# Kernel tuning notes

Hardware: AMD Instinct MI355X
Metric: run time of the kernel (lower is better)

## Reference

```python
import jax, jax.numpy as jnp
from jax import lax
import numpy as np

LATENT_DIM = 128
NUM_SAMPLES = 524288
STEPS = 30


def setup_inputs() -> dict:
    key = jax.random.key(0)
    kW, = jax.random.split(key, 1)
    h = jnp.zeros((LATENT_DIM,), dtype=jnp.float32)
    W = jax.random.normal(kW, (LATENT_DIM, LATENT_DIM), dtype=jnp.float32) * 0.001
    return {"h": h, "W": W, "num_samples": NUM_SAMPLES, "steps": STEPS}


def reference(h, W, num_samples, steps):
    # Block Gibbs sampling chain of the RBM: z <- Bernoulli(sigmoid(h + z @ W))
    latent_dim = h.shape[0]
    key = jax.random.key(42)
    k_init, k_loop = jax.random.split(key)
    # initial state: uniform {0,1} bits, matching torch.randint(0, 2, ...)
    z0 = jax.random.randint(k_init, (num_samples, latent_dim), 0, 2).astype(jnp.float32)
    step_keys = jax.random.split(k_loop, steps)

    def gibbs_step(z, k):
        probs = jax.nn.sigmoid(h + z @ W)            # [num_samples, latent_dim]
        u = jax.random.uniform(k, z.shape, dtype=z.dtype)
        z_new = (u < probs).astype(z.dtype)
        return z_new, None

    z_final, _ = lax.scan(gibbs_step, z0, step_keys)
    return z_final
```

## Files before the change

kernel.cpp:

```cpp
#include <hip/hip_runtime.h>
#include <cstdint>
#include <utility>


constexpr int LATENT = 128;
constexpr int NS = 524288;
constexpr int STEPS = 30;
constexpr int R = 4;
constexpr int TPB = 1024;
constexpr int WAVES_PB = TPB / 64;
constexpr int NWAVES = NS / R;
constexpr int NBLOCKS = NWAVES / WAVES_PB;

typedef float f32x2 __attribute__((ext_vector_type(2)));

template <typename F, int... I>
__device__ __forceinline__ void unroll_impl(F&& f, std::integer_sequence<int, I...>) {
  (f(std::integral_constant<int, I>{}), ...);
}
template <int N, typename F>
__device__ __forceinline__ void unroll_n(F&& f) {
  unroll_impl(static_cast<F&&>(f), std::make_integer_sequence<int, N>{});
}

struct TFOut { uint32_t a, b; };

__host__ __device__ constexpr TFOut tf2x32_ct(uint32_t k0, uint32_t k1,
                                              uint32_t x0, uint32_t x1) {
  const uint32_t ks2 = k0 ^ k1 ^ 0x1BD11BDAu;
  x0 += k0; x1 += k1;
#define TFR(r) { x0 += x1; x1 = (x1 << (r)) | (x1 >> (32 - (r))); x1 ^= x0; }
  TFR(13) TFR(15) TFR(26) TFR(6)
  x0 += k1;  x1 += ks2 + 1u;
  TFR(17) TFR(29) TFR(16) TFR(24)
  x0 += ks2; x1 += k0 + 2u;
  TFR(13) TFR(15) TFR(26) TFR(6)
  x0 += k0;  x1 += k1 + 3u;
  TFR(17) TFR(29) TFR(16) TFR(24)
  x0 += k1;  x1 += ks2 + 4u;
  TFR(13) TFR(15) TFR(26) TFR(6)
  x0 += ks2; x1 += k0 + 5u;
#undef TFR
  return {x0, x1};
}

__device__ __forceinline__ uint32_t rotl_hw(uint32_t x, int r) {
  return __builtin_amdgcn_alignbit(x, x, (uint32_t)(32 - r));
}
__device__ __forceinline__ TFOut tf2x32_dev(uint32_t k0, uint32_t k1,
                                            uint32_t x0, uint32_t x1) {
  const uint32_t ks2 = k0 ^ k1 ^ 0x1BD11BDAu;
  x0 += k0; x1 += k1;
#define TFRD(r) { x0 += x1; x1 = rotl_hw(x1, r); x1 ^= x0; }
  TFRD(13) TFRD(15) TFRD(26) TFRD(6)
  x0 += k1;  x1 += ks2 + 1u;
  TFRD(17) TFRD(29) TFRD(16) TFRD(24)
  x0 += ks2; x1 += k0 + 2u;
  TFRD(13) TFRD(15) TFRD(26) TFRD(6)
  x0 += k0;  x1 += k1 + 3u;
  TFRD(17) TFRD(29) TFRD(16) TFRD(24)
  x0 += k1;  x1 += ks2 + 4u;
  TFRD(13) TFRD(15) TFRD(26) TFRD(6)
  x0 += ks2; x1 += k0 + 5u;
#undef TFRD
  return {x0, x1};
}

struct Keys { uint32_t sk[62]; };
constexpr Keys make_keys() {
  Keys K{};
  const TFOut ki = tf2x32_ct(0u, 42u, 0u, 0u);
  const TFOut kl = tf2x32_ct(0u, 42u, 0u, 1u);
  const TFOut k2 = tf2x32_ct(ki.a, ki.b, 0u, 1u);
  K.sk[60] = k2.a; K.sk[61] = k2.b;
  for (uint32_t t = 0; t < (uint32_t)STEPS; ++t) {
    const TFOut s = tf2x32_ct(kl.a, kl.b, 0u, t);
    K.sk[2 * t] = s.a; K.sk[2 * t + 1] = s.b;
  }
  return K;
}
__constant__ Keys KC = make_keys();

__device__ __forceinline__ uint32_t rbits(uint32_t ka, uint32_t kb, uint32_t c) {
  const TFOut r = tf2x32_dev(ka, kb, 0u, c);
  return r.a ^ r.b;
}

__device__ __forceinline__ float bits_to_u(uint32_t b) {
  return __fsub_rn(__uint_as_float((b >> 9) | 0x3f800000u), 1.0f);
}

__device__ __forceinline__ float ref_sigmoid(float v) {
  float a = -v;
  float y = __fadd_rn(__fmul_rn(a, 1.9875691500E-4f), 1.3981999507E-3f);
  y = __fadd_rn(__fmul_rn(y, a), 8.3334519073E-3f);
  y = __fadd_rn(__fmul_rn(y, a), 4.1665795894E-2f);
  y = __fadd_rn(__fmul_rn(y, a), 1.6666665459E-1f);
  y = __fadd_rn(__fmul_rn(y, a), 5.0000001201E-1f);
  float a2 = __fmul_rn(a, a);
  y = __fadd_rn(__fmul_rn(y, a2), a);
  float e = __fadd_rn(1.0f, y);
  return __fdiv_rn(1.0f, __fadd_rn(1.0f, e));
}

__device__ __forceinline__ void ballot_scalar(int pred, uint32_t& lo, uint32_t& hi) {
  const unsigned long long b = __ballot(pred);
  lo = __builtin_amdgcn_readfirstlane((uint32_t)b);
  hi = __builtin_amdgcn_readfirstlane((uint32_t)(b >> 32));
}

template <int B>
__device__ __forceinline__ uint64_t sel_bit2(uint32_t mask, uint64_t one2) {
  uint64_t f2;
  asm("s_bitcmp1_b32 %1, %3\n\t"
      "s_cselect_b64 %0, %2, 0"
      : "=s"(f2) : "s"(mask), "s"(one2), "n"(B) : "scc");
  return f2;
}

__device__ __forceinline__ void pk_fma_pair(f32x2& acc, uint64_t f2, f32x2 w) {
  asm("v_pk_fma_f32 %0, %2, %1, %0"
      : "+v"(acc) : "v"(w), "s"(f2));
}

__global__ __launch_bounds__(TPB, 8)
void rbm_gibbs_kernel(const float* __restrict__ h, const float* __restrict__ W,
                      float* __restrict__ out) {
  __shared__ f32x2 WsA[64 * 64];
  __shared__ f32x2 WsB[64 * 64];

  const int tid = threadIdx.x;
  {
    const float2* Wg2 = reinterpret_cast<const float2*>(W);
    #pragma unroll
    for (int it = 0; it < 4096 / TPB; ++it) {
      const int idx = it * TPB + tid;
      const int m = idx >> 6, l = idx & 63;
      const float2 g0 = Wg2[(2 * m) * 64 + l];
      const float2 g1 = Wg2[(2 * m + 1) * 64 + l];
      WsA[idx] = f32x2{g0.x, g0.y};
      WsB[idx] = f32x2{g1.x, g1.y};
    }
  }
  __syncthreads();

  const int lane = tid & 63;
  const int wid  = blockIdx.x * WAVES_PB + (tid >> 6);
  const uint32_t cb = (uint32_t)wid * (uint32_t)(R * LATENT);
  const int j0 = 2 * lane;
  const float h0 = h[j0], h1 = h[j0 + 1];
  const uint64_t one2 = 0x3f8000003f800000ull;

  uint32_t mElo[R], mEhi[R], mOlo[R], mOhi[R];
  {
    const uint32_t ka = KC.sk[60], kb = KC.sk[61];
    #pragma unroll
    for (int q = 0; q < R; ++q) {
      const uint32_t c = cb + (uint32_t)(q * LATENT) + (uint32_t)j0;
      ballot_scalar((int)(rbits(ka, kb, c) & 1u),      mElo[q], mEhi[q]);
      ballot_scalar((int)(rbits(ka, kb, c + 1u) & 1u), mOlo[q], mOhi[q]);
    }
  }

  #pragma unroll 1
  for (int t = 0; t < STEPS; ++t) {
    f32x2 acc[R];
    #pragma unroll
    for (int q = 0; q < R; ++q) acc[q] = f32x2{0.f, 0.f};

    unroll_n<32>([&](auto MC) {
      constexpr int m = MC.value;
      const f32x2 wA = WsA[m * 64 + lane];
      const f32x2 wB = WsB[m * 64 + lane];
      #pragma unroll
      for (int q = 0; q < R; ++q) {
        pk_fma_pair(acc[q], sel_bit2<m>(mElo[q], one2), wA);
        pk_fma_pair(acc[q], sel_bit2<m>(mOlo[q], one2), wB);
      }
    });
    unroll_n<32>([&](auto MC) {
      constexpr int m = MC.value;
      const f32x2 wA = WsA[(m + 32) * 64 + lane];
      const f32x2 wB = WsB[(m + 32) * 64 + lane];
      #pragma unroll
      for (int q = 0; q < R; ++q) {
        pk_fma_pair(acc[q], sel_bit2<m>(mEhi[q], one2), wA);
        pk_fma_pair(acc[q], sel_bit2<m>(mOhi[q], one2), wB);
      }
    });

    const uint32_t sa = KC.sk[2 * t], sb = KC.sk[2 * t + 1];
    #pragma unroll
    for (int q = 0; q < R; ++q) {
      const uint32_t c = cb + (uint32_t)(q * LATENT) + (uint32_t)j0;
      const uint32_t uE = rbits(sa, sb, c);
      const uint32_t uO = rbits(sa, sb, c + 1u);
      const float pE = ref_sigmoid(__fadd_rn(h0, acc[q].x));
      const float pO = ref_sigmoid(__fadd_rn(h1, acc[q].y));
      ballot_scalar((int)(bits_to_u(uE) < pE), mElo[q], mEhi[q]);
      ballot_scalar((int)(bits_to_u(uO) < pO), mOlo[q], mOhi[q]);
    }
  }

  float2* out2 = reinterpret_cast<float2*>(out);
  #pragma unroll
  for (int q = 0; q < R; ++q) {
    float2 z;
    z.x = (float)(((lane < 32 ? mElo[q] : mEhi[q]) >> (lane & 31)) & 1u);
    z.y = (float)(((lane < 32 ? mOlo[q] : mOhi[q]) >> (lane & 31)) & 1u);
    out2[(size_t)(wid * R + q) * 64 + lane] = z;
  }
}

extern "C" void kernel_launch(void* const* d_in, const int* in_sizes, int n_in,
                              void* d_out, int out_size, void* d_ws, size_t ws_size,
                              hipStream_t stream) {
  const float* h = (const float*)d_in[0];
  const float* W = (const float*)d_in[1];
  float* out = (float*)d_out;
  rbm_gibbs_kernel<<<NBLOCKS, TPB, 0, stream>>>(h, W, out);
}
```

Before: 10.54 ms.

## Map one sample row per thread with per-thread bit masks instead of wave ballots

Replaces the wave-cooperative layout (4 rows per wave, lanes own column pairs, state bits shared via ballot into scalar registers, packed FMA with scalar-selected weights) with one sample row per thread. Each thread keeps its 128-bit state in four registers and loops over columns in chunks of 16, converting each bit to a float and doing scalar FMAs against W rows read from LDS as broadcast float4 loads. This drops the ballots and readfirstlane calls but gives up the scalar-operand packed-FMA trick. It also adds per-bit float conversions, non-unrolled inner loops and a strided per-thread output store, so the inner loop may become LDS- and VALU-bound.

```diff
diff --git a/kernel.cpp b/kernel.cpp
--- a/kernel.cpp
+++ b/kernel.cpp
@@ -1,27 +1,14 @@
 #include <hip/hip_runtime.h>
 #include <cstdint>
-#include <utility>
 
 
 constexpr int LATENT = 128;
 constexpr int NS = 524288;
 constexpr int STEPS = 30;
-constexpr int R = 4;
 constexpr int TPB = 1024;
-constexpr int WAVES_PB = TPB / 64;
-constexpr int NWAVES = NS / R;
-constexpr int NBLOCKS = NWAVES / WAVES_PB;
-
-typedef float f32x2 __attribute__((ext_vector_type(2)));
-
-template <typename F, int... I>
-__device__ __forceinline__ void unroll_impl(F&& f, std::integer_sequence<int, I...>) {
-  (f(std::integral_constant<int, I>{}), ...);
-}
-template <int N, typename F>
-__device__ __forceinline__ void unroll_n(F&& f) {
-  unroll_impl(static_cast<F&&>(f), std::make_integer_sequence<int, N>{});
-}
+constexpr int NBLOCKS = NS / TPB;
+
+typedef float f32x4 __attribute__((ext_vector_type(4)));
 
 struct TFOut { uint32_t a, b; };
 
@@ -103,112 +90,118 @@
   return __fdiv_rn(1.0f, __fadd_rn(1.0f, e));
 }
 
-__device__ __forceinline__ void ballot_scalar(int pred, uint32_t& lo, uint32_t& hi) {
-  const unsigned long long b = __ballot(pred);
-  lo = __builtin_amdgcn_readfirstlane((uint32_t)b);
-  hi = __builtin_amdgcn_readfirstlane((uint32_t)(b >> 32));
-}
-
-template <int B>
-__device__ __forceinline__ uint64_t sel_bit2(uint32_t mask, uint64_t one2) {
-  uint64_t f2;
-  asm("s_bitcmp1_b32 %1, %3\n\t"
-      "s_cselect_b64 %0, %2, 0"
-      : "=s"(f2) : "s"(mask), "s"(one2), "n"(B) : "scc");
-  return f2;
-}
-
-__device__ __forceinline__ void pk_fma_pair(f32x2& acc, uint64_t f2, f32x2 w) {
-  asm("v_pk_fma_f32 %0, %2, %1, %0"
-      : "+v"(acc) : "v"(w), "s"(f2));
-}
-
-__global__ __launch_bounds__(TPB, 8)
+__global__ __launch_bounds__(TPB, 4)
 void rbm_gibbs_kernel(const float* __restrict__ h, const float* __restrict__ W,
                       float* __restrict__ out) {
-  __shared__ f32x2 WsA[64 * 64];
-  __shared__ f32x2 WsB[64 * 64];
+  __shared__ float Ws[LATENT * LATENT];
+  __shared__ float hs[LATENT];
 
   const int tid = threadIdx.x;
   {
-    const float2* Wg2 = reinterpret_cast<const float2*>(W);
+    const float4* Wg = reinterpret_cast<const float4*>(W);
+    float4* Wl = reinterpret_cast<float4*>(Ws);
     #pragma unroll
-    for (int it = 0; it < 4096 / TPB; ++it) {
-      const int idx = it * TPB + tid;
-      const int m = idx >> 6, l = idx & 63;
-      const float2 g0 = Wg2[(2 * m) * 64 + l];
-      const float2 g1 = Wg2[(2 * m + 1) * 64 + l];
-      WsA[idx] = f32x2{g0.x, g0.y};
-      WsB[idx] = f32x2{g1.x, g1.y};
-    }
-  }
+    for (int p = 0; p < 4096 / TPB; ++p)
+      Wl[p * TPB + tid] = Wg[p * TPB + tid];
+  }
+  if (tid < LATENT) hs[tid] = h[tid];
   __syncthreads();
 
-  const int lane = tid & 63;
-  const int wid  = blockIdx.x * WAVES_PB + (tid >> 6);
-  const uint32_t cb = (uint32_t)wid * (uint32_t)(R * LATENT);
-  const int j0 = 2 * lane;
-  const float h0 = h[j0], h1 = h[j0 + 1];
-  const uint64_t one2 = 0x3f8000003f800000ull;
-
-  uint32_t mElo[R], mEhi[R], mOlo[R], mOhi[R];
+  const uint32_t row = (uint32_t)blockIdx.x * TPB + (uint32_t)tid;
+  const uint32_t cb = row << 7;
+
+  uint32_t z0r, z1r, z2r, z3r;
   {
     const uint32_t ka = KC.sk[60], kb = KC.sk[61];
+    uint32_t zd[4];
     #pragma unroll
-    for (int q = 0; q < R; ++q) {
-      const uint32_t c = cb + (uint32_t)(q * LATENT) + (uint32_t)j0;
-      ballot_scalar((int)(rbits(ka, kb, c) & 1u),      mElo[q], mEhi[q]);
-      ballot_scalar((int)(rbits(ka, kb, c + 1u) & 1u), mOlo[q], mOhi[q]);
+    for (int dw = 0; dw < 4; ++dw) {
+      uint32_t acc = 0;
+      const uint32_t c0 = cb + (uint32_t)(dw * 32);
+      #pragma unroll 1
+      for (uint32_t i = 0; i < 32u; ++i)
+        acc |= (rbits(ka, kb, c0 + i) & 1u) << i;
+      zd[dw] = acc;
     }
-  }
+    z0r = zd[0]; z1r = zd[1]; z2r = zd[2]; z3r = zd[3];
+  }
+
+  const f32x4* Ws4 = reinterpret_cast<const f32x4*>(Ws);
 
   #pragma unroll 1
   for (int t = 0; t < STEPS; ++t) {
-    f32x2 acc[R];
-    #pragma unroll
-    for (int q = 0; q < R; ++q) acc[q] = f32x2{0.f, 0.f};
-
-    unroll_n<32>([&](auto MC) {
-      constexpr int m = MC.value;
-      const f32x2 wA = WsA[m * 64 + lane];
-      const f32x2 wB = WsB[m * 64 + lane];
+    const uint32_t sa = KC.sk[2 * t], sb = KC.sk[2 * t + 1];
+    uint32_t zn0 = 0, zn1 = 0, zn2 = 0, zn3 = 0;
+
+    #pragma unroll 1
+    for (int jc = 0; jc < 8; ++jc) {
+      float acc[16];
       #pragma unroll
-      for (int q = 0; q < R; ++q) {
-        pk_fma_pair(acc[q], sel_bit2<m>(mElo[q], one2), wA);
-        pk_fma_pair(acc[q], sel_bit2<m>(mOlo[q], one2), wB);
+      for (int i = 0; i < 16; ++i) acc[i] = 0.f;
+
+      const f32x4* Wp = Ws4 + jc * 4;
+      #pragma unroll
+      for (int dw = 0; dw < 4; ++dw) {
+        const uint32_t zd = (dw == 0) ? z0r : (dw == 1) ? z1r : (dw == 2) ? z2r : z3r;
+        #pragma unroll 1
+        for (int u = 0; u < 32; ++u) {
+          const int k = dw * 32 + u;
+          const float zf = (float)((zd >> u) & 1u);
+          const f32x4 wA = Wp[k * 32 + 0];
+          const f32x4 wB = Wp[k * 32 + 1];
+          const f32x4 wC = Wp[k * 32 + 2];
+          const f32x4 wD = Wp[k * 32 + 3];
+          acc[ 0] = __fmaf_rn(zf, wA.x, acc[ 0]);
+          acc[ 1] = __fmaf_rn(zf, wA.y, acc[ 1]);
+          acc[ 2] = __fmaf_rn(zf, wA.z, acc[ 2]);
+          acc[ 3] = __fmaf_rn(zf, wA.w, acc[ 3]);
+          acc[ 4] = __fmaf_rn(zf, wB.x, acc[ 4]);
+          acc[ 5] = __fmaf_rn(zf, wB.y, acc[ 5]);
+          acc[ 6] = __fmaf_rn(zf, wB.z, acc[ 6]);
+          acc[ 7] = __fmaf_rn(zf, wB.w, acc[ 7]);
+          acc[ 8] = __fmaf_rn(zf, wC.x, acc[ 8]);
+          acc[ 9] = __fmaf_rn(zf, wC.y, acc[ 9]);
+          acc[10] = __fmaf_rn(zf, wC.z, acc[10]);
+          acc[11] = __fmaf_rn(zf, wC.w, acc[11]);
+          acc[12] = __fmaf_rn(zf, wD.x, acc[12]);
+          acc[13] = __fmaf_rn(zf, wD.y, acc[13]);
+          acc[14] = __fmaf_rn(zf, wD.z, acc[14]);
+          acc[15] = __fmaf_rn(zf, wD.w, acc[15]);
+        }
       }
-    });
-    unroll_n<32>([&](auto MC) {
-      constexpr int m = MC.value;
-      const f32x2 wA = WsA[(m + 32) * 64 + lane];
-      const f32x2 wB = WsB[(m + 32) * 64 + lane];
+
+      const uint32_t cbase = cb + (uint32_t)(jc * 16);
+      uint32_t zc = 0;
       #pragma unroll
-      for (int q = 0; q < R; ++q) {
-        pk_fma_pair(acc[q], sel_bit2<m>(mEhi[q], one2), wA);
-        pk_fma_pair(acc[q], sel_bit2<m>(mOhi[q], one2), wB);
+      for (int i = 0; i < 16; ++i) {
+        const float logit = __fadd_rn(hs[jc * 16 + i], acc[i]);
+        const float p = ref_sigmoid(logit);
+        const float uf = bits_to_u(rbits(sa, sb, cbase + (uint32_t)i));
+        zc |= (uf < p ? 1u : 0u) << i;
       }
-    });
-
-    const uint32_t sa = KC.sk[2 * t], sb = KC.sk[2 * t + 1];
-    #pragma unroll
-    for (int q = 0; q < R; ++q) {
-      const uint32_t c = cb + (uint32_t)(q * LATENT) + (uint32_t)j0;
-      const uint32_t uE = rbits(sa, sb, c);
-      const uint32_t uO = rbits(sa, sb, c + 1u);
-      const float pE = ref_sigmoid(__fadd_rn(h0, acc[q].x));
-      const float pO = ref_sigmoid(__fadd_rn(h1, acc[q].y));
-      ballot_scalar((int)(bits_to_u(uE) < pE), mElo[q], mEhi[q]);
-      ballot_scalar((int)(bits_to_u(uO) < pO), mOlo[q], mOhi[q]);
+
+      const uint32_t sv = zc << ((jc & 1) * 16);
+      zn0 |= ((jc >> 1) == 0) ? sv : 0u;
+      zn1 |= ((jc >> 1) == 1) ? sv : 0u;
+      zn2 |= ((jc >> 1) == 2) ? sv : 0u;
+      zn3 |= ((jc >> 1) == 3) ? sv : 0u;
     }
-  }
-
-  float2* out2 = reinterpret_cast<float2*>(out);
+    z0r = zn0; z1r = zn1; z2r = zn2; z3r = zn3;
+  }
+
+  float4* out4 = reinterpret_cast<float4*>(out) + (size_t)row * 32;
   #pragma unroll
-  for (int q = 0; q < R; ++q) {
-    float2 z;
-    z.x = (float)(((lane < 32 ? mElo[q] : mEhi[q]) >> (lane & 31)) & 1u);
-    z.y = (float)(((lane < 32 ? mOlo[q] : mOhi[q]) >> (lane & 31)) & 1u);
-    out2[(size_t)(wid * R + q) * 64 + lane] = z;
+  for (int dw = 0; dw < 4; ++dw) {
+    const uint32_t zd = (dw == 0) ? z0r : (dw == 1) ? z1r : (dw == 2) ? z2r : z3r;
+    #pragma unroll 1
+    for (int q = 0; q < 8; ++q) {
+      float4 v;
+      v.x = (float)((zd >> (q * 4 + 0)) & 1u);
+      v.y = (float)((zd >> (q * 4 + 1)) & 1u);
+      v.z = (float)((zd >> (q * 4 + 2)) & 1u);
+      v.w = (float)((zd >> (q * 4 + 3)) & 1u);
+      out4[dw * 8 + q] = v;
+    }
   }
 }
 
```

Result: slower. 10.92 ms (+3.6%).
